# Kernel optimization log

Hardware: AMD Instinct MI355X
Metric: run time of the kernel (lower is better)

The kernel has to match this reference:

```python
import jax, jax.numpy as jnp
import numpy as np

P, Q, R = 3, 1, 0          # CliffordAlgebra(p=3, q=1, r=0)
N = P + Q + R
ALG = 1 << N               # 16 basis blades
SHIFTS = (1, 2, 4)


def _cayley():
    """Cayley table C[i,j,k]: blade_i * blade_j = C[i,j,i^j] * blade_{i^j}."""
    metric = [1.0] * P + [-1.0] * Q + [0.0] * R
    C = np.zeros((ALG, ALG, ALG), np.float32)
    for a in range(ALG):
        for b in range(ALG):
            x = a >> 1
            s = 0
            while x:                       # reordering sign
                s += bin(x & b).count('1')
                x >>= 1
            val = -1.0 if (s & 1) else 1.0
            for i in range(N):             # metric for repeated basis vectors
                if (a & b) >> i & 1:
                    val *= metric[i]
            C[a, b, a ^ b] = val
    return C

_C = _cayley()
C0 = jnp.asarray(_C[:, :, 0])                        # grade-0 slice: <a*b>_0
A = jnp.asarray((_C - _C.transpose(1, 0, 2)) / 2.0)  # antisym: (ab - ba)/2
VEC_MASK = jnp.asarray(np.array([1.0 if bin(i).count('1') == 1 else 0.0 for i in range(ALG)], np.float32))
BIV_MASK = jnp.asarray(np.array([1.0 if bin(i).count('1') == 2 else 0.0 for i in range(ALG)], np.float32))


def setup_inputs() -> dict:
    key = jax.random.key(0)
    k1, k2 = jax.random.split(key, 2)
    B, T, D = 8, 4096, 1024
    return {
        "x": jax.random.normal(k1, (B, T, D), jnp.float32),
        "gate_w": jax.random.normal(k2, (D, 1), jnp.float32) * 0.02,
        "gate_b": jnp.zeros((1,), jnp.float32),
        "scalar_weight": jnp.float32(0.5),
        "bivector_weight": jnp.float32(0.5),
    }


def reference(x, gate_w, gate_b, scalar_weight, bivector_weight):
    B, T, D = x.shape
    n = D // ALG                         # 64 chunks of 16 (D divisible, no pad)
    ss = jax.nn.sigmoid(scalar_weight)
    sb = jax.nn.sigmoid(bivector_weight)
    gate = jax.nn.sigmoid(x @ gate_w + gate_b)   # (B,T,1), gate of x (loop-invariant)
    xc = x.reshape(B, T, n, ALG)
    out = x
    for shift in SHIFTS:                 # T=4096 > shift always
        c = x - jnp.roll(x, shift, axis=1)
        cc = c.reshape(B, T, n, ALG)
        # inner product: scalar part per chunk, summed over chunks
        scalar = jnp.einsum('btni,btnj,ij->bt', xc, cc, C0)
        # wedge: antisymmetrized geometric product of vector-grade projections
        av = xc * VEC_MASK
        bv = cc * VEC_MASK
        wedge = jnp.einsum('btni,btnj,ijk->btnk', av, bv, A) * BIV_MASK
        delta = (sb * wedge).reshape(B, T, D)
        delta = delta.at[..., 0].add(ss * scalar)   # scalar_part lives at index 0
        out = out + gate * delta
    return out
```

## Files before the change

kernel.cpp:

```cpp
#include <hip/hip_runtime.h>
#include <math.h>


constexpr int T_DIM   = 4096;
constexpr int D_DIM   = 1024;
constexpr int L_STRIP = 16;
constexpr int PF      = 3;
constexpr int WARM    = 4;

constexpr int QB0 = 0x8000;
constexpr int QB1 = 0x8055;
constexpr int QB2 = 0x80AA;

template <int PAT>
__device__ __forceinline__ float swz(float v) {
    return __int_as_float(__builtin_amdgcn_ds_swizzle(__float_as_int(v), PAT));
}

__device__ __forceinline__ float sigmoidf(float z) {
    return 1.0f / (1.0f + __expf(-z));
}

__global__ __launch_bounds__(256, 6) void clifford_kernel(
    const float* __restrict__ x,
    const float* __restrict__ gate_w,
    const float* __restrict__ gate_b,
    const float* __restrict__ scalar_w,
    const float* __restrict__ bivec_w,
    float* __restrict__ out,
    int nstrips)
{
    int blk = blockIdx.x;
    if ((gridDim.x & 7) == 0) {
        const int per = gridDim.x >> 3;
        blk = (blockIdx.x & 7) * per + (blockIdx.x >> 3);
    }
    if (blk >= nstrips) return;

    const int tid  = threadIdx.x;
    const int wid  = tid >> 6;
    const int lane = tid & 63;
    const int sub  = tid & 3;

    const int spb = T_DIM / L_STRIP;
    const int b   = blk / spb;
    const int t0  = (blk - b * spb) * L_STRIP;

    const int col = tid << 2;
    const float* __restrict__ xb = x   + ((size_t)b * T_DIM) * D_DIM + col;
    float*       __restrict__ ob = out + ((size_t)b * T_DIM + t0) * D_DIM + col;

    __shared__ float red[2][4][2];

    float4 s[8];
    #pragma unroll
    for (int j = 0; j < WARM + PF; ++j) {
        const int trow = (t0 - WARM + j) & (T_DIM - 1);
        s[(j + 4) & 7] = *(const float4*)(xb + (size_t)trow * D_DIM);
    }
    const float4 gv = *(const float4*)(gate_w + col);

    const float ss = sigmoidf(scalar_w[0]);
    const float sb = sigmoidf(bivec_w[0]);
    const float gb = gate_b[0];

    float4 ws;
    if      (sub == 0) ws = make_float4( 1.f,  1.f,  1.f, -1.f);
    else if (sub == 1) ws = make_float4( 1.f, -1.f, -1.f, -1.f);
    else if (sub == 2) ws = make_float4(-1.f,  1.f,  1.f,  1.f);
    else               ws = make_float4( 1.f,  1.f,  1.f, -1.f);
    const float m3  = (sub == 0) ? 1.f : 0.f;
    const float a1  = (sub == 1) ? 1.f : 0.f;
    const float a2  = (sub == 2) ? 1.f : 0.f;
    const float m12 = (sub == 3) ? 1.f : 0.f;

    #pragma unroll
    for (int k = 0; k < L_STRIP; ++k) {
        if (k + PF < L_STRIP) {
            s[(k + PF) & 7] = *(const float4*)(xb + (size_t)(t0 + k + PF) * D_DIM);
        }

        const float4 cur = s[k & 7];
        const float4 p1  = s[(k + 7) & 7];
        const float4 p2  = s[(k + 6) & 7];
        const float4 p4  = s[(k + 4) & 7];

        float4 cs;
        cs.x = 3.f * cur.x - p1.x - p2.x - p4.x;
        cs.y = 3.f * cur.y - p1.y - p2.y - p4.y;
        cs.z = 3.f * cur.z - p1.z - p2.z - p4.z;
        cs.w = 3.f * cur.w - p1.w - p2.w - p4.w;

        float gp = cur.x * gv.x + cur.y * gv.y + cur.z * gv.z + cur.w * gv.w;
        float sc = ws.x * (cur.x * cs.x) + ws.y * (cur.y * cs.y)
                 + ws.z * (cur.z * cs.z) + ws.w * (cur.w * cs.w);

        const float x1  = swz<QB0>(cur.y), x2  = swz<QB0>(cur.z);
        const float x4b = swz<QB1>(cur.x), x8b = swz<QB2>(cur.x);
        const float c1  = swz<QB0>(cs.y),  c2  = swz<QB0>(cs.z);
        const float c4b = swz<QB1>(cs.x),  c8b = swz<QB2>(cs.x);

        const float w3  = x1 * c2  - x2  * c1;
        const float w5  = x1 * c4b - x4b * c1;
        const float w6  = x2 * c4b - x4b * c2;
        const float w9  = x1 * c8b - x8b * c1;
        const float w10 = x2 * c8b - x8b * c2;
        const float w12 = x4b * c8b - x8b * c4b;

        const float4 dl = make_float4(m12 * w12,
                                      a1 * w5 + a2 * w9,
                                      a1 * w6 + a2 * w10,
                                      m3 * w3);

        #pragma unroll
        for (int o = 32; o > 0; o >>= 1) {
            gp += __shfl_xor(gp, o, 64);
            sc += __shfl_xor(sc, o, 64);
        }

        const int par = k & 1;
        if (lane == 0) { red[par][wid][0] = gp; red[par][wid][1] = sc; }
        __syncthreads();
        float gsum = 0.f, scsum = 0.f;
        #pragma unroll
        for (int i = 0; i < 4; ++i) {
            gsum  += red[par][i][0];
            scsum += red[par][i][1];
        }

        const float gate = sigmoidf(gsum + gb);
        const float gsb  = gate * sb;

        float4 o4;
        o4.x = cur.x + gsb * dl.x;
        o4.y = cur.y + gsb * dl.y;
        o4.z = cur.z + gsb * dl.z;
        o4.w = cur.w + gsb * dl.w;
        if (tid == 0) o4.x += gate * ss * scsum;
        *(float4*)(ob + (size_t)k * D_DIM) = o4;
    }
}

extern "C" void kernel_launch(void* const* d_in, const int* in_sizes, int n_in,
                              void* d_out, int out_size, void* d_ws, size_t ws_size,
                              hipStream_t stream) {
    const float* x  = (const float*)d_in[0];
    const float* gw = (const float*)d_in[1];
    const float* gb = (const float*)d_in[2];
    const float* sw = (const float*)d_in[3];
    const float* bw = (const float*)d_in[4];
    float* out = (float*)d_out;

    const int BT      = in_sizes[0] / D_DIM;
    const int nstrips = BT / L_STRIP;
    hipLaunchKernelGGL(clifford_kernel, dim3(nstrips), dim3(256), 0, stream,
                       x, gw, gb, sw, bw, out, nstrips);
}
```

Baseline: 255.0 us.

## Assign one wavefront per time strip to remove block-level barrier reductions

Each 64-lane wavefront now handles a full 1024-wide row strip, with each lane holding four float4 columns, instead of spreading one row across a 256-thread block. The gate and scalar reductions then finish with wave shuffles alone, which removes the shared-memory exchange and the __syncthreads on every time step. In exchange each thread holds four times as many registers (a 32-entry float4 ring buffer), so the launch bound drops to 2 and occupancy falls, which may reduce latency hiding for this memory-bound kernel.

```diff
diff --git a/kernel.cpp b/kernel.cpp
--- a/kernel.cpp
+++ b/kernel.cpp
@@ -21,7 +21,7 @@
     return 1.0f / (1.0f + __expf(-z));
 }
 
-__global__ __launch_bounds__(256, 6) void clifford_kernel(
+__global__ __launch_bounds__(256, 2) void clifford_kernel(
     const float* __restrict__ x,
     const float* __restrict__ gate_w,
     const float* __restrict__ gate_b,
@@ -35,30 +35,33 @@
         const int per = gridDim.x >> 3;
         blk = (blockIdx.x & 7) * per + (blockIdx.x >> 3);
     }
-    if (blk >= nstrips) return;
 
-    const int tid  = threadIdx.x;
-    const int wid  = tid >> 6;
-    const int lane = tid & 63;
-    const int sub  = tid & 3;
+    const int lane  = threadIdx.x & 63;
+    const int strip = blk * 4 + (threadIdx.x >> 6);
+    if (strip >= nstrips) return;
 
     const int spb = T_DIM / L_STRIP;
-    const int b   = blk / spb;
-    const int t0  = (blk - b * spb) * L_STRIP;
+    const int b   = strip / spb;
+    const int t0  = (strip - b * spb) * L_STRIP;
+    const int sub = lane & 3;
+    const int coff = lane << 2;
 
-    const int col = tid << 2;
-    const float* __restrict__ xb = x   + ((size_t)b * T_DIM) * D_DIM + col;
-    float*       __restrict__ ob = out + ((size_t)b * T_DIM + t0) * D_DIM + col;
+    const float* __restrict__ xb = x + (size_t)b * T_DIM * D_DIM;
+    float*       __restrict__ ob = out + ((size_t)b * T_DIM + t0) * D_DIM;
 
-    __shared__ float red[2][4][2];
-
-    float4 s[8];
+    float4 s[8][4];
     #pragma unroll
     for (int j = 0; j < WARM + PF; ++j) {
         const int trow = (t0 - WARM + j) & (T_DIM - 1);
-        s[(j + 4) & 7] = *(const float4*)(xb + (size_t)trow * D_DIM);
+        const float* __restrict__ r = xb + (size_t)trow * D_DIM + coff;
+        #pragma unroll
+        for (int m = 0; m < 4; ++m)
+            s[(j + 4) & 7][m] = *(const float4*)(r + (m << 8));
     }
-    const float4 gv = *(const float4*)(gate_w + col);
+    float4 gv[4];
+    #pragma unroll
+    for (int m = 0; m < 4; ++m)
+        gv[m] = *(const float4*)(gate_w + coff + (m << 8));
 
     const float ss = sigmoidf(scalar_w[0]);
     const float sb = sigmoidf(bivec_w[0]);
@@ -77,67 +80,72 @@
     #pragma unroll
     for (int k = 0; k < L_STRIP; ++k) {
         if (k + PF < L_STRIP) {
-            s[(k + PF) & 7] = *(const float4*)(xb + (size_t)(t0 + k + PF) * D_DIM);
+            const float* __restrict__ r =
+                xb + (size_t)(t0 + k + PF) * D_DIM + coff;
+            #pragma unroll
+            for (int m = 0; m < 4; ++m)
+                s[(k + PF) & 7][m] = *(const float4*)(r + (m << 8));
         }
 
-        const float4 cur = s[k & 7];
-        const float4 p1  = s[(k + 7) & 7];
-        const float4 p2  = s[(k + 6) & 7];
-        const float4 p4  = s[(k + 4) & 7];
+        float gp = 0.f, sc = 0.f;
+        float4 dl[4];
 
-        float4 cs;
-        cs.x = 3.f * cur.x - p1.x - p2.x - p4.x;
-        cs.y = 3.f * cur.y - p1.y - p2.y - p4.y;
-        cs.z = 3.f * cur.z - p1.z - p2.z - p4.z;
-        cs.w = 3.f * cur.w - p1.w - p2.w - p4.w;
+        #pragma unroll
+        for (int m = 0; m < 4; ++m) {
+            const float4 cur = s[k & 7][m];
+            const float4 p1  = s[(k + 7) & 7][m];
+            const float4 p2  = s[(k + 6) & 7][m];
+            const float4 p4  = s[(k + 4) & 7][m];
 
-        float gp = cur.x * gv.x + cur.y * gv.y + cur.z * gv.z + cur.w * gv.w;
-        float sc = ws.x * (cur.x * cs.x) + ws.y * (cur.y * cs.y)
-                 + ws.z * (cur.z * cs.z) + ws.w * (cur.w * cs.w);
+            float4 cs;
+            cs.x = 3.f * cur.x - p1.x - p2.x - p4.x;
+            cs.y = 3.f * cur.y - p1.y - p2.y - p4.y;
+            cs.z = 3.f * cur.z - p1.z - p2.z - p4.z;
+            cs.w = 3.f * cur.w - p1.w - p2.w - p4.w;
 
-        const float x1  = swz<QB0>(cur.y), x2  = swz<QB0>(cur.z);
-        const float x4b = swz<QB1>(cur.x), x8b = swz<QB2>(cur.x);
-        const float c1  = swz<QB0>(cs.y),  c2  = swz<QB0>(cs.z);
-        const float c4b = swz<QB1>(cs.x),  c8b = swz<QB2>(cs.x);
+            gp += cur.x * gv[m].x + cur.y * gv[m].y
+                + cur.z * gv[m].z + cur.w * gv[m].w;
+            sc += ws.x * (cur.x * cs.x) + ws.y * (cur.y * cs.y)
+                + ws.z * (cur.z * cs.z) + ws.w * (cur.w * cs.w);
 
-        const float w3  = x1 * c2  - x2  * c1;
-        const float w5  = x1 * c4b - x4b * c1;
-        const float w6  = x2 * c4b - x4b * c2;
-        const float w9  = x1 * c8b - x8b * c1;
-        const float w10 = x2 * c8b - x8b * c2;
-        const float w12 = x4b * c8b - x8b * c4b;
+            const float x1  = swz<QB0>(cur.y), x2  = swz<QB0>(cur.z);
+            const float x4b = swz<QB1>(cur.x), x8b = swz<QB2>(cur.x);
+            const float c1  = swz<QB0>(cs.y),  c2  = swz<QB0>(cs.z);
+            const float c4b = swz<QB1>(cs.x),  c8b = swz<QB2>(cs.x);
 
-        const float4 dl = make_float4(m12 * w12,
-                                      a1 * w5 + a2 * w9,
-                                      a1 * w6 + a2 * w10,
-                                      m3 * w3);
+            const float w3  = x1 * c2  - x2  * c1;
+            const float w5  = x1 * c4b - x4b * c1;
+            const float w6  = x2 * c4b - x4b * c2;
+            const float w9  = x1 * c8b - x8b * c1;
+            const float w10 = x2 * c8b - x8b * c2;
+            const float w12 = x4b * c8b - x8b * c4b;
+
+            dl[m] = make_float4(m12 * w12,
+                                a1 * w5 + a2 * w9,
+                                a1 * w6 + a2 * w10,
+                                m3 * w3);
+        }
 
         #pragma unroll
         for (int o = 32; o > 0; o >>= 1) {
             gp += __shfl_xor(gp, o, 64);
             sc += __shfl_xor(sc, o, 64);
         }
-
-        const int par = k & 1;
-        if (lane == 0) { red[par][wid][0] = gp; red[par][wid][1] = sc; }
-        __syncthreads();
-        float gsum = 0.f, scsum = 0.f;
-        #pragma unroll
-        for (int i = 0; i < 4; ++i) {
-            gsum  += red[par][i][0];
-            scsum += red[par][i][1];
-        }
-
-        const float gate = sigmoidf(gsum + gb);
+        const float gate = sigmoidf(gp + gb);
         const float gsb  = gate * sb;
 
-        float4 o4;
-        o4.x = cur.x + gsb * dl.x;
-        o4.y = cur.y + gsb * dl.y;
-        o4.z = cur.z + gsb * dl.z;
-        o4.w = cur.w + gsb * dl.w;
-        if (tid == 0) o4.x += gate * ss * scsum;
-        *(float4*)(ob + (size_t)k * D_DIM) = o4;
+        float* __restrict__ orow = ob + (size_t)k * D_DIM + coff;
+        #pragma unroll
+        for (int m = 0; m < 4; ++m) {
+            const float4 cur = s[k & 7][m];
+            float4 o4;
+            o4.x = cur.x + gsb * dl[m].x;
+            o4.y = cur.y + gsb * dl[m].y;
+            o4.z = cur.z + gsb * dl[m].z;
+            o4.w = cur.w + gsb * dl[m].w;
+            if (m == 0 && lane == 0) o4.x += gate * ss * sc;
+            *(float4*)(orow + (m << 8)) = o4;
+        }
     }
 }
 
@@ -153,6 +161,7 @@
 
     const int BT      = in_sizes[0] / D_DIM;
     const int nstrips = BT / L_STRIP;
-    hipLaunchKernelGGL(clifford_kernel, dim3(nstrips), dim3(256), 0, stream,
+    const int blocks  = (nstrips + 3) / 4;
+    hipLaunchKernelGGL(clifford_kernel, dim3(blocks), dim3(256), 0, stream,
                        x, gw, gb, sw, bw, out, nstrips);
 }
```

New measurement: 246.3 us. 3.4% less time.
